# Performance work log

Hardware: AMD Instinct MI355X
Metric: run time of the kernel (lower is better)

Reference implementation:

```python
import jax, jax.numpy as jnp
import numpy as np

EPSILON = 1e-8
MAX_WEIGHT = 0.15
N_ITER = 20
STEP_SIZE = 0.05
B, P = 32768, 45


def _simplex_projection(w):
    # clamp + renormalize, done twice (differentiable approximation)
    w = jnp.clip(w, 0.0, MAX_WEIGHT)
    w = w / (jnp.sum(w, axis=-1, keepdims=True) + EPSILON)
    w = jnp.clip(w, 0.0, MAX_WEIGHT)
    w = w / (jnp.sum(w, axis=-1, keepdims=True) + EPSILON)
    return w


def setup_inputs() -> dict:
    key = jax.random.key(0)
    k1, k2 = jax.random.split(key, 2)
    # SPD-ish covariance for a well-behaved iterative solve
    A = jax.random.normal(k1, (B, P, P), dtype=jnp.float32) * 0.1
    sigma = jnp.einsum('bij,bkj->bik', A, A) + 0.1 * jnp.eye(P, dtype=jnp.float32)
    beta = jax.nn.softmax(jax.random.normal(k2, (B, P), dtype=jnp.float32), axis=-1)
    w_prev = jnp.full((B, P), 1.0 / P, dtype=jnp.float32)
    return {
        'sigma': sigma,
        'beta': beta,
        'w_prev': w_prev,
        'log_lambda_sparse': jnp.asarray(-3.0, dtype=jnp.float32),
        'log_lambda_turnover': jnp.asarray(-2.0, dtype=jnp.float32),
    }


def reference(sigma, beta, w_prev, log_lambda_sparse, log_lambda_turnover):
    Bb, Pp = beta.shape
    lam_s = jnp.exp(log_lambda_sparse)
    lam_t = jnp.exp(log_lambda_turnover)
    w0 = jnp.full((Bb, Pp), 1.0 / Pp, dtype=sigma.dtype)

    def step(w, _):
        Sw = jnp.einsum('bij,bj->bi', sigma, w)  # [B,P]
        grad = 2.0 * Sw - beta + lam_s * jnp.sign(w) + 2.0 * lam_t * (w - w_prev)
        w = _simplex_projection(w - STEP_SIZE * grad)
        return w, None

    w, _ = jax.lax.scan(step, w0, None, length=N_ITER)
    return w
```

## Files before the change

kernel.cpp:

```cpp
#include <hip/hip_runtime.h>
#include <math.h>

#define P 45
#define N_ITER 20

typedef float v2f __attribute__((ext_vector_type(2)));
typedef float v4f __attribute__((ext_vector_type(4)));

template<int CTRL>
__device__ __forceinline__ float dpp_add(float x) {
    int xi = __builtin_bit_cast(int, x);
    int yi = __builtin_amdgcn_update_dpp(0, xi, CTRL, 0xF, 0xF, true);
    return x + __builtin_bit_cast(float, yi);
}

__device__ __forceinline__ float wave_sum_bcast(float x) {
    x = dpp_add<0x111>(x);
    x = dpp_add<0x112>(x);
    x = dpp_add<0x114>(x);
    x = dpp_add<0x118>(x);
    x = dpp_add<0x142>(x);
    x = dpp_add<0x143>(x);
    int si = __builtin_amdgcn_readlane(__builtin_bit_cast(int, x), 63);
    return __builtin_bit_cast(float, si);
}

__device__ __forceinline__ float clamp015(float x) {
    return __builtin_amdgcn_fmed3f(x, 0.0f, 0.15f);
}

__global__ __launch_bounds__(64) void drb_kernel(
    const float* __restrict__ sigma,
    const float* __restrict__ beta,
    const float* __restrict__ w_prev,
    const float* __restrict__ lls,
    const float* __restrict__ llt,
    float* __restrict__ out)
{
    const int b    = blockIdx.x;
    const int lane = threadIdx.x;
    const bool active = lane < P;

    const float lam_s  = expf(lls[0]);
    const float lam_t2 = 2.0f * expf(llt[0]);

    float base = 0.0f;
    if (active) {
        base = -beta[(size_t)b * P + lane]
               - lam_t2 * w_prev[(size_t)b * P + lane];
    }

    const int cidx = active ? lane : 0;
    const float* sp = sigma + (size_t)b * (P * P) + cidx;
    float rv[P + 1];
    #pragma unroll
    for (int j = 0; j < P; ++j) {
        float v = sp[(size_t)j * P];
        rv[j] = active ? v : 0.0f;
    }
    rv[P] = 0.0f;
    const bool ones = (lane == P);
    v2f row2[23];
    #pragma unroll
    for (int k = 0; k < 23; ++k) {
        float lo = ones ? 1.0f : rv[2 * k];
        float hi = (2 * k + 1 < P) ? (ones ? 1.0f : rv[2 * k + 1]) : 0.0f;
        v2f t; t.x = lo; t.y = hi;
        row2[k] = t;
    }
    #pragma unroll
    for (int k = 0; k < 23; ++k) asm volatile("" : "+v"(row2[k]));

    __shared__ __align__(16) float sh[128];

    float c = active ? (float)(1.0 / 45.0) : 0.0f;

    for (int it = 0; it < N_ITER; ++it) {
        float* shb = sh + ((it & 1) << 6);
        shb[lane] = c;
        __syncthreads();
        const v4f* shv = (const v4f*)shb;

        v2f acc0; acc0.x = 0.0f; acc0.y = 0.0f;
        v2f acc1 = acc0, acc2 = acc0;
        #pragma unroll
        for (int k = 0; k < 11; ++k) {
            v4f q = shv[k];
            v2f lo; lo.x = q.x; lo.y = q.y;
            v2f hi; hi.x = q.z; hi.y = q.w;
            acc0 = __builtin_elementwise_fma(row2[2 * k],     lo, acc0);
            acc1 = __builtin_elementwise_fma(row2[2 * k + 1], hi, acc1);
        }
        {
            v4f q = shv[11];
            v2f lo; lo.x = q.x; lo.y = q.y;
            acc2 = __builtin_elementwise_fma(row2[22], lo, acc2);
        }
        v2f am = acc0 + acc1;
        am = am + acc2;
        const float acc = am.x + am.y;

        const float s2 = __builtin_bit_cast(float,
            __builtin_amdgcn_readlane(__builtin_bit_cast(int, acc), P));
        const float r = __builtin_amdgcn_rcpf(s2 + 1e-8f);

        const float t = c * r;
        float g = fmaf(lam_t2, t, base);
        g += (c > 0.0f) ? lam_s : 0.0f;
        g = fmaf(r + r, acc, g);
        const float x = fmaf(-0.05f, g, t);

        const float a  = clamp015(x);
        const float s1 = wave_sum_bcast(a);
        const float r1 = __builtin_amdgcn_rcpf(s1 + 1e-8f);
        c = clamp015(a * r1);
    }

    const float sf = wave_sum_bcast(c);
    const float rf = __builtin_amdgcn_rcpf(sf + 1e-8f);
    if (active) out[(size_t)b * P + lane] = c * rf;
}

extern "C" void kernel_launch(void* const* d_in, const int* in_sizes, int n_in,
                              void* d_out, int out_size, void* d_ws, size_t ws_size,
                              hipStream_t stream) {
    const float* sigma  = (const float*)d_in[0];
    const float* beta   = (const float*)d_in[1];
    const float* w_prev = (const float*)d_in[2];
    const float* lls    = (const float*)d_in[3];
    const float* llt    = (const float*)d_in[4];
    float* out = (float*)d_out;

    const int B = in_sizes[1] / P;
    drb_kernel<<<B, 64, 0, stream>>>(sigma, beta, w_prev, lls, llt, out);
}
```

Measured before the change: 377.2 us.

## Split matvec broadcast between LDS vector reads and readlane scalar operands

New measurement: 387.5 us. +2.7%, slower.

```diff
diff --git a/kernel.cpp b/kernel.cpp
--- a/kernel.cpp
+++ b/kernel.cpp
@@ -40,6 +40,7 @@
     const int b    = blockIdx.x;
     const int lane = threadIdx.x;
     const bool active = lane < P;
+    const bool ones   = (lane == P);
 
     const float lam_s  = expf(lls[0]);
     const float lam_t2 = 2.0f * expf(llt[0]);
@@ -52,53 +53,62 @@
 
     const int cidx = active ? lane : 0;
     const float* sp = sigma + (size_t)b * (P * P) + cidx;
-    float rv[P + 1];
+
+    v2f rowA[12];
     #pragma unroll
-    for (int j = 0; j < P; ++j) {
-        float v = sp[(size_t)j * P];
-        rv[j] = active ? v : 0.0f;
+    for (int k = 0; k < 12; ++k) {
+        float lo = sp[(size_t)(2 * k)     * P];
+        float hi = sp[(size_t)(2 * k + 1) * P];
+        v2f t;
+        t.x = active ? lo : (ones ? 1.0f : 0.0f);
+        t.y = active ? hi : (ones ? 1.0f : 0.0f);
+        rowA[k] = t;
     }
-    rv[P] = 0.0f;
-    const bool ones = (lane == P);
-    v2f row2[23];
+    float rowB[21];
     #pragma unroll
-    for (int k = 0; k < 23; ++k) {
-        float lo = ones ? 1.0f : rv[2 * k];
-        float hi = (2 * k + 1 < P) ? (ones ? 1.0f : rv[2 * k + 1]) : 0.0f;
-        v2f t; t.x = lo; t.y = hi;
-        row2[k] = t;
+    for (int k = 0; k < 21; ++k) {
+        float v = sp[(size_t)(24 + k) * P];
+        rowB[k] = active ? v : (ones ? 1.0f : 0.0f);
     }
     #pragma unroll
-    for (int k = 0; k < 23; ++k) asm volatile("" : "+v"(row2[k]));
+    for (int k = 0; k < 12; ++k) asm volatile("" : "+v"(rowA[k]));
+    #pragma unroll
+    for (int k = 0; k < 21; ++k) asm volatile("" : "+v"(rowB[k]));
 
     __shared__ __align__(16) float sh[128];
 
     float c = active ? (float)(1.0 / 45.0) : 0.0f;
 
+    #pragma unroll
     for (int it = 0; it < N_ITER; ++it) {
         float* shb = sh + ((it & 1) << 6);
         shb[lane] = c;
-        __syncthreads();
+
+        const int ci = __builtin_bit_cast(int, c);
+        float accB0 = 0.0f, accB1 = 0.0f, accB2 = 0.0f;
+        #pragma unroll
+        for (int k = 0; k < 21; k += 3) {
+            float w0 = __builtin_bit_cast(float, __builtin_amdgcn_readlane(ci, 24 + k));
+            float w1 = __builtin_bit_cast(float, __builtin_amdgcn_readlane(ci, 25 + k));
+            float w2 = __builtin_bit_cast(float, __builtin_amdgcn_readlane(ci, 26 + k));
+            accB0 = fmaf(rowB[k],     w0, accB0);
+            accB1 = fmaf(rowB[k + 1], w1, accB1);
+            accB2 = fmaf(rowB[k + 2], w2, accB2);
+        }
+
         const v4f* shv = (const v4f*)shb;
-
-        v2f acc0; acc0.x = 0.0f; acc0.y = 0.0f;
-        v2f acc1 = acc0, acc2 = acc0;
+        v2f accA0; accA0.x = 0.0f; accA0.y = 0.0f;
+        v2f accA1 = accA0;
         #pragma unroll
-        for (int k = 0; k < 11; ++k) {
+        for (int k = 0; k < 6; ++k) {
             v4f q = shv[k];
             v2f lo; lo.x = q.x; lo.y = q.y;
             v2f hi; hi.x = q.z; hi.y = q.w;
-            acc0 = __builtin_elementwise_fma(row2[2 * k],     lo, acc0);
-            acc1 = __builtin_elementwise_fma(row2[2 * k + 1], hi, acc1);
+            accA0 = __builtin_elementwise_fma(rowA[2 * k],     lo, accA0);
+            accA1 = __builtin_elementwise_fma(rowA[2 * k + 1], hi, accA1);
         }
-        {
-            v4f q = shv[11];
-            v2f lo; lo.x = q.x; lo.y = q.y;
-            acc2 = __builtin_elementwise_fma(row2[22], lo, acc2);
-        }
-        v2f am = acc0 + acc1;
-        am = am + acc2;
-        const float acc = am.x + am.y;
+        v2f amA = accA0 + accA1;
+        const float acc = (amA.x + amA.y) + ((accB0 + accB1) + accB2);
 
         const float s2 = __builtin_bit_cast(float,
             __builtin_amdgcn_readlane(__builtin_bit_cast(int, acc), P));
```
